# Optimization experiments

Hardware: AMD Instinct MI355X
Metric: run time of the kernel (lower is better)

## Reference

```python
import jax, jax.numpy as jnp
import numpy as np

NUM_HEADS = 16
WINDOW = 256
DIM = 1024


def setup_inputs() -> dict:
    key = jax.random.key(0)
    k1, k2, k3, k4, k5 = jax.random.split(key, 5)
    B, L, D = 2, 2048, DIM
    s = 1.0 / np.sqrt(D)
    return {
        "x": jax.random.normal(k1, (B, L, D), dtype=jnp.float32),
        "in_proj_w": jax.random.uniform(k2, (3 * D, D), dtype=jnp.float32, minval=-s, maxval=s),
        "in_proj_b": jax.random.uniform(k3, (3 * D,), dtype=jnp.float32, minval=-s, maxval=s),
        "out_w": jax.random.uniform(k4, (D, D), dtype=jnp.float32, minval=-s, maxval=s),
        "out_b": jax.random.uniform(k5, (D,), dtype=jnp.float32, minval=-s, maxval=s),
    }


def reference(x, in_proj_w, in_proj_b, out_w, out_b):
    B, L, D = x.shape
    H = NUM_HEADS
    hd = D // H

    # combined qkv projection, as in nn.MultiheadAttention
    qkv = x @ in_proj_w.T + in_proj_b          # [B, L, 3D]
    q, k, v = jnp.split(qkv, 3, axis=-1)
    q = q.reshape(B, L, H, hd).transpose(0, 2, 1, 3)  # [B, H, L, hd]
    k = k.reshape(B, L, H, hd).transpose(0, 2, 1, 3)
    v = v.reshape(B, L, H, hd).transpose(0, 2, 1, 3)

    scale = 1.0 / jnp.sqrt(jnp.asarray(hd, dtype=x.dtype))
    scores = jnp.einsum("bhqd,bhkd->bhqk", q * scale, k)  # [B, H, L, L]

    # sliding-window causal mask: allowed iff i-window < j <= i
    i = jnp.arange(L)[:, None]
    j = jnp.arange(L)[None, :]
    allowed = (j <= i) & (j > i - WINDOW)                  # [L, L]
    scores = jnp.where(allowed[None, None], scores, -jnp.inf)

    attn = jax.nn.softmax(scores, axis=-1)
    out = jnp.einsum("bhqk,bhkd->bhqd", attn, v)           # [B, H, L, hd]
    out = out.transpose(0, 2, 1, 3).reshape(B, L, D)
    return out @ out_w.T + out_b
```

## Files before the change

### kernel.cpp

```cpp
#include <hip/hip_runtime.h>


#define SEQ_L 2048
#define WIN   256

typedef __bf16 bf16x8 __attribute__((ext_vector_type(8)));
typedef float  f32x4  __attribute__((ext_vector_type(4)));

__device__ __forceinline__ unsigned short f32_to_bf16(float f) {
  unsigned int u = __float_as_uint(f);
  u += 0x7FFFu + ((u >> 16) & 1u);
  return (unsigned short)(u >> 16);
}

__device__ __forceinline__ void async16(const unsigned short* g, unsigned short* l) {
  __builtin_amdgcn_global_load_lds(
      (const __attribute__((address_space(1))) unsigned int*)g,
      (__attribute__((address_space(3))) unsigned int*)l, 16, 0, 0);
}

__global__ void cast_all(const float* __restrict__ x,  unsigned short* __restrict__ xo,
                         const float* __restrict__ w1, unsigned short* __restrict__ w1o,
                         const float* __restrict__ w2, unsigned short* __restrict__ w2o) {
  int i = blockIdx.x * 256 + threadIdx.x;
  const float* in; unsigned short* out; int k;
  if (i < 1048576)       { in = x;  out = xo;  k = i; }
  else if (i < 1835008)  { in = w1; out = w1o; k = i - 1048576; }
  else                   { in = w2; out = w2o; k = i - 1835008; }
  float4 v = ((const float4*)in)[k];
  ushort4 o;
  o.x = f32_to_bf16(v.x); o.y = f32_to_bf16(v.y);
  o.z = f32_to_bf16(v.z); o.w = f32_to_bf16(v.w);
  ((ushort4*)out)[k] = o;
}

template<int TBM, int TBN, int MI, int NI, int OUTBF>
__global__ __launch_bounds__(256) void gemm_nt(
    const unsigned short* __restrict__ A,
    const unsigned short* __restrict__ Bt,
    const float* __restrict__ bias,
    void* __restrict__ Cout, int M, int N, int K)
{
  __shared__ unsigned short As[TBM * 64];
  __shared__ unsigned short Bs[TBN * 64];

  const int tid  = threadIdx.x;
  const int lane = tid & 63;
  const int wave = tid >> 6;
  const int wr   = (wave >> 1) * (MI * 16);
  const int wc   = (wave & 1) * (NI * 16);
  const int quad = lane >> 4;
  const int l16  = lane & 15;
  const int lrow = lane >> 3;
  const int scol = (lane & 7) ^ lrow;

  const long m0 = (long)blockIdx.y * TBM;
  const long n0 = (long)blockIdx.x * TBN;

  f32x4 acc[MI][NI];
#pragma unroll
  for (int i = 0; i < MI; ++i)
#pragma unroll
    for (int j = 0; j < NI; ++j)
#pragma unroll
      for (int r = 0; r < 4; ++r) acc[i][j][r] = 0.0f;

  for (int k0 = 0; k0 < K; k0 += 64) {
#pragma unroll
    for (int p = 0; p < TBM / 32; ++p) {
      int rb = wave * (TBM / 4) + p * 8;
      async16(A + (m0 + rb + lrow) * (long)K + k0 + scol * 8, &As[rb * 64]);
    }
#pragma unroll
    for (int p = 0; p < TBN / 32; ++p) {
      int rb = wave * (TBN / 4) + p * 8;
      async16(Bt + (n0 + rb + lrow) * (long)K + k0 + scol * 8, &Bs[rb * 64]);
    }
    __syncthreads();
#pragma unroll
    for (int ks = 0; ks < 2; ++ks) {
      bf16x8 af[MI], bfv[NI];
#pragma unroll
      for (int mi = 0; mi < MI; ++mi) {
        int r = wr + mi * 16 + l16;
        af[mi] = *(const bf16x8*)(&As[r * 64 + ((ks * 4 + quad) ^ (r & 7)) * 8]);
      }
#pragma unroll
      for (int ni = 0; ni < NI; ++ni) {
        int r = wc + ni * 16 + l16;
        bfv[ni] = *(const bf16x8*)(&Bs[r * 64 + ((ks * 4 + quad) ^ (r & 7)) * 8]);
      }
#pragma unroll
      for (int mi = 0; mi < MI; ++mi)
#pragma unroll
        for (int ni = 0; ni < NI; ++ni)
          acc[mi][ni] = __builtin_amdgcn_mfma_f32_16x16x32_bf16(af[mi], bfv[ni], acc[mi][ni], 0, 0, 0);
    }
    __syncthreads();
  }

#pragma unroll
  for (int ni = 0; ni < NI; ++ni) {
    long col = n0 + wc + ni * 16 + l16;
    float bv = bias[col];
#pragma unroll
    for (int mi = 0; mi < MI; ++mi) {
      long rowb = m0 + wr + mi * 16 + quad * 4;
#pragma unroll
      for (int r = 0; r < 4; ++r) {
        float v = acc[mi][ni][r] + bv;
        if (OUTBF) ((unsigned short*)Cout)[(rowb + r) * N + col] = f32_to_bf16(v);
        else       ((float*)Cout)[(rowb + r) * N + col] = v;
      }
    }
  }
}

__global__ __launch_bounds__(256) void attn_kernel(
    const unsigned short* __restrict__ qkv,
    unsigned short* __restrict__ aout)
{
  __shared__ unsigned short Ks[64 * 72];
  __shared__ unsigned short Vt[64 * 72];
  __shared__ unsigned short Ps[4 * 16 * 72];

  const int tid  = threadIdx.x;
  const int w    = tid >> 6;
  const int lane = tid & 63;
  const int quad = lane >> 4;
  const int l16  = lane & 15;

  const int blk = blockIdx.x;
  const int qb  = blk & 15;
  const int h   = (blk >> 4) & 15;
  const int b   = blk >> 8;

  const int  i0 = qb * 128;
  const long rowbase = (long)b * SEQ_L;

  bf16x8 aq[2][2];
#pragma unroll
  for (int sub = 0; sub < 2; ++sub) {
    const unsigned short* qp =
        qkv + (rowbase + i0 + sub * 64 + w * 16 + l16) * 3072 + h * 64 + quad * 8;
    aq[sub][0] = *(const bf16x8*)(qp);
    aq[sub][1] = *(const bf16x8*)(qp + 32);
  }

  f32x4 o[2][4];
  float l_i[2][4];
#pragma unroll
  for (int sub = 0; sub < 2; ++sub)
#pragma unroll
    for (int ni = 0; ni < 4; ++ni)
#pragma unroll
      for (int r = 0; r < 4; ++r) { o[sub][ni][r] = 0.0f; l_i[sub][r] = 0.0f; }

  unsigned short* psw = &Ps[w * 16 * 72];

  const int j_begin = (i0 >= WIN) ? i0 - WIN : 0;

  for (int j0 = j_begin; j0 < i0 + 128; j0 += 64) {
    __syncthreads();
#pragma unroll
    for (int p = 0; p < 2; ++p) {
      int c = p * 256 + tid, row = c >> 3, col8 = c & 7;
      const unsigned short* base = qkv + (rowbase + j0 + row) * 3072 + h * 64 + col8 * 8;
      *(uint4*)(&Ks[row * 72 + col8 * 8]) = *(const uint4*)(base + 1024);
      unsigned short tmp[8];
      *(uint4*)tmp = *(const uint4*)(base + 2048);
      int rsw = row ^ (col8 << 3);
#pragma unroll
      for (int e = 0; e < 8; ++e)
        Vt[(col8 * 8 + e) * 72 + rsw] = tmp[e];
    }
    __syncthreads();

    bf16x8 kf[4][2];
#pragma unroll
    for (int g = 0; g < 4; ++g) {
      kf[g][0] = *(const bf16x8*)(&Ks[(g * 16 + l16) * 72 + quad * 8]);
      kf[g][1] = *(const bf16x8*)(&Ks[(g * 16 + l16) * 72 + 32 + quad * 8]);
    }
    bf16x8 vf[2][4];
#pragma unroll
    for (int kk = 0; kk < 2; ++kk)
#pragma unroll
      for (int ni = 0; ni < 4; ++ni) {
        int d  = ni * 16 + l16;
        int rb = (kk * 32 + quad * 8) ^ (((d >> 3) & 7) << 3);
        vf[kk][ni] = *(const bf16x8*)(&Vt[d * 72 + rb]);
      }

#pragma unroll
    for (int sub = 0; sub < 2; ++sub) {
      const int i0s = i0 + sub * 64 + w * 16;
      if (j0 > i0s + 15) continue;
      if (j0 + 63 + WIN <= i0s) continue;

      f32x4 s[4];
#pragma unroll
      for (int g = 0; g < 4; ++g) {
        f32x4 z;
#pragma unroll
        for (int r = 0; r < 4; ++r) z[r] = 0.0f;
        z = __builtin_amdgcn_mfma_f32_16x16x32_bf16(aq[sub][0], kf[g][0], z, 0, 0, 0);
        z = __builtin_amdgcn_mfma_f32_16x16x32_bf16(aq[sub][1], kf[g][1], z, 0, 0, 0);
        s[g] = z;
      }
#pragma unroll
      for (int g = 0; g < 4; ++g) {
        int j = j0 + g * 16 + l16;
#pragma unroll
        for (int r = 0; r < 4; ++r) {
          int i = i0s + quad * 4 + r;
          bool ok = (j <= i) && (j > i - WIN);
          float e = ok ? __expf(s[g][r] * 0.125f) : 0.0f;
          psw[(quad * 4 + r) * 72 + g * 16 + l16] = f32_to_bf16(e);
          l_i[sub][r] += e;
        }
      }
      asm volatile("s_waitcnt lgkmcnt(0)" ::: "memory");
#pragma unroll
      for (int kk = 0; kk < 2; ++kk) {
        bf16x8 ap = *(const bf16x8*)(&psw[l16 * 72 + kk * 32 + quad * 8]);
#pragma unroll
        for (int ni = 0; ni < 4; ++ni)
          o[sub][ni] = __builtin_amdgcn_mfma_f32_16x16x32_bf16(ap, vf[kk][ni], o[sub][ni], 0, 0, 0);
      }
    }
  }

#pragma unroll
  for (int sub = 0; sub < 2; ++sub)
#pragma unroll
    for (int r = 0; r < 4; ++r) {
      float rs = l_i[sub][r];
      rs += __shfl_xor(rs, 1);
      rs += __shfl_xor(rs, 2);
      rs += __shfl_xor(rs, 4);
      rs += __shfl_xor(rs, 8);
      float inv_l = 1.0f / rs;
      long row = rowbase + i0 + sub * 64 + w * 16 + quad * 4 + r;
#pragma unroll
      for (int ni = 0; ni < 4; ++ni)
        aout[row * 1024 + h * 64 + ni * 16 + l16] = f32_to_bf16(o[sub][ni][r] * inv_l);
    }
}

extern "C" void kernel_launch(void* const* d_in, const int* in_sizes, int n_in,
                              void* d_out, int out_size, void* d_ws, size_t ws_size,
                              hipStream_t stream)
{
  const float* x  = (const float*)d_in[0];
  const float* w1 = (const float*)d_in[1];
  const float* b1 = (const float*)d_in[2];
  const float* w2 = (const float*)d_in[3];
  const float* b2 = (const float*)d_in[4];
  float* out = (float*)d_out;

  char* ws = (char*)d_ws;
  unsigned short* x_bf   = (unsigned short*)(ws);
  unsigned short* w1_bf  = (unsigned short*)(ws + 8388608);
  unsigned short* w2_bf  = (unsigned short*)(ws + 14680064);
  unsigned short* qkv_bf = (unsigned short*)(ws + 16777216);
  unsigned short* at_bf  = (unsigned short*)(ws + 41943040);

  cast_all<<<8192, 256, 0, stream>>>(x, x_bf, w1, w1_bf, w2, w2_bf);

  dim3 g1(3072 / 128, 4096 / 128);
  gemm_nt<128, 128, 4, 4, 1><<<g1, 256, 0, stream>>>(x_bf, w1_bf, b1, qkv_bf, 4096, 3072, 1024);

  attn_kernel<<<512, 256, 0, stream>>>(qkv_bf, at_bf);

  dim3 g2(1024 / 64, 4096 / 64);
  gemm_nt<64, 64, 2, 2, 0><<<g2, 256, 0, stream>>>(at_bf, w2_bf, b2, out, 4096, 1024, 1024);
}
```

Measured before the change: 164.1 us.

## Split-K output GEMM, skip masked tiles, MFMA row sums, exp2 and cheaper bf16 rounding

Replaces the output projection with a new 128x64 kernel that splits K across two wave pairs and reduces the partial sums through shared memory. In attention, fully masked 16-column tiles skip their MFMAs and write zeros, fully visible tiles skip the mask test, exp is computed as exp2 with a folded constant, and the row-sum reduction becomes an MFMA against a vector of ones. The bf16 conversion now rounds half-up instead of round-to-nearest-even. These changes aim to cut ALU, shuffle and GEMM scheduling cost, at the price of slightly different rounding and summing the bf16-rounded probabilities rather than the fp32 ones.

```diff
diff --git a/kernel.cpp b/kernel.cpp
--- a/kernel.cpp
+++ b/kernel.cpp
@@ -8,9 +8,7 @@
 typedef float  f32x4  __attribute__((ext_vector_type(4)));
 
 __device__ __forceinline__ unsigned short f32_to_bf16(float f) {
-  unsigned int u = __float_as_uint(f);
-  u += 0x7FFFu + ((u >> 16) & 1u);
-  return (unsigned short)(u >> 16);
+  return (unsigned short)((__float_as_uint(f) + 0x8000u) >> 16);
 }
 
 __device__ __forceinline__ void async16(const unsigned short* g, unsigned short* l) {
@@ -116,6 +114,101 @@
   }
 }
 
+__global__ __launch_bounds__(256) void gemm_nt_sk(
+    const unsigned short* __restrict__ A,
+    const unsigned short* __restrict__ Bt,
+    const float* __restrict__ bias,
+    float* __restrict__ C, int M, int N, int K)
+{
+  __shared__ unsigned short As[2][128 * 64];
+  __shared__ unsigned short Bs[2][64 * 64];
+
+  const int tid  = threadIdx.x;
+  const int lane = tid & 63;
+  const int wave = tid >> 6;
+  const int half = wave >> 1;
+  const int rh   = wave & 1;
+  const int quad = lane >> 4;
+  const int l16  = lane & 15;
+  const int lrow = lane >> 3;
+  const int scol = (lane & 7) ^ lrow;
+
+  const long m0 = (long)blockIdx.y * 128;
+  const long n0 = (long)blockIdx.x * 64;
+  const int  kh = half * (K / 2);
+
+  f32x4 acc[4][4];
+#pragma unroll
+  for (int i = 0; i < 4; ++i)
+#pragma unroll
+    for (int j = 0; j < 4; ++j)
+#pragma unroll
+      for (int r = 0; r < 4; ++r) acc[i][j][r] = 0.0f;
+
+  for (int it = 0; it < K / 2; it += 64) {
+    const int k0 = kh + it;
+#pragma unroll
+    for (int p = 0; p < 8; ++p) {
+      int rb = rh * 64 + p * 8;
+      async16(A + (m0 + rb + lrow) * (long)K + k0 + scol * 8, &As[half][rb * 64]);
+    }
+#pragma unroll
+    for (int p = 0; p < 4; ++p) {
+      int rb = rh * 32 + p * 8;
+      async16(Bt + (n0 + rb + lrow) * (long)K + k0 + scol * 8, &Bs[half][rb * 64]);
+    }
+    __syncthreads();
+#pragma unroll
+    for (int ks = 0; ks < 2; ++ks) {
+      bf16x8 af[4], bfv[4];
+#pragma unroll
+      for (int mi = 0; mi < 4; ++mi) {
+        int r = rh * 64 + mi * 16 + l16;
+        af[mi] = *(const bf16x8*)(&As[half][r * 64 + ((ks * 4 + quad) ^ (r & 7)) * 8]);
+      }
+#pragma unroll
+      for (int ni = 0; ni < 4; ++ni) {
+        int r = ni * 16 + l16;
+        bfv[ni] = *(const bf16x8*)(&Bs[half][r * 64 + ((ks * 4 + quad) ^ (r & 7)) * 8]);
+      }
+#pragma unroll
+      for (int mi = 0; mi < 4; ++mi)
+#pragma unroll
+        for (int ni = 0; ni < 4; ++ni)
+          acc[mi][ni] = __builtin_amdgcn_mfma_f32_16x16x32_bf16(af[mi], bfv[ni], acc[mi][ni], 0, 0, 0);
+    }
+    __syncthreads();
+  }
+
+  float* Cs = (float*)As;
+  if (half == 1) {
+#pragma unroll
+    for (int mi = 0; mi < 4; ++mi)
+#pragma unroll
+      for (int ni = 0; ni < 4; ++ni) {
+        int slot = ((mi * 4 + ni) * 4 + quad) * 16 + l16;
+        *(f32x4*)&Cs[rh * 4096 + slot * 4] = acc[mi][ni];
+      }
+  }
+  __syncthreads();
+  if (half == 0) {
+#pragma unroll
+    for (int ni = 0; ni < 4; ++ni) {
+      long col = n0 + ni * 16 + l16;
+      float bv = bias[col];
+#pragma unroll
+      for (int mi = 0; mi < 4; ++mi) {
+        int slot = ((mi * 4 + ni) * 4 + quad) * 16 + l16;
+        f32x4 part = *(const f32x4*)&Cs[rh * 4096 + slot * 4];
+        long rowb = m0 + rh * 64 + mi * 16 + quad * 4;
+#pragma unroll
+        for (int r = 0; r < 4; ++r)
+          C[(rowb + r) * N + col] = acc[mi][ni][r] + part[r] + bv;
+      }
+    }
+  }
+}
+
 __global__ __launch_bounds__(256) void attn_kernel(
     const unsigned short* __restrict__ qkv,
     unsigned short* __restrict__ aout)
@@ -137,6 +230,11 @@
 
   const int  i0 = qb * 128;
   const long rowbase = (long)b * SEQ_L;
+  const float C_EXP = 0.18033688f;
+
+  bf16x8 ones;
+#pragma unroll
+  for (int e = 0; e < 8; ++e) ones[e] = (__bf16)1.0f;
 
   bf16x8 aq[2][2];
 #pragma unroll
@@ -147,17 +245,18 @@
     aq[sub][1] = *(const bf16x8*)(qp + 32);
   }
 
-  f32x4 o[2][4];
-  float l_i[2][4];
-#pragma unroll
-  for (int sub = 0; sub < 2; ++sub)
+  f32x4 o[2][4], ol[2];
+#pragma unroll
+  for (int sub = 0; sub < 2; ++sub) {
+#pragma unroll
+    for (int r = 0; r < 4; ++r) ol[sub][r] = 0.0f;
 #pragma unroll
     for (int ni = 0; ni < 4; ++ni)
 #pragma unroll
-      for (int r = 0; r < 4; ++r) { o[sub][ni][r] = 0.0f; l_i[sub][r] = 0.0f; }
+      for (int r = 0; r < 4; ++r) o[sub][ni][r] = 0.0f;
+  }
 
   unsigned short* psw = &Ps[w * 16 * 72];
-
   const int j_begin = (i0 >= WIN) ? i0 - WIN : 0;
 
   for (int j0 = j_begin; j0 < i0 + 128; j0 += 64) {
@@ -198,32 +297,42 @@
       if (j0 > i0s + 15) continue;
       if (j0 + 63 + WIN <= i0s) continue;
 
-      f32x4 s[4];
 #pragma unroll
       for (int g = 0; g < 4; ++g) {
+        const int jmin = j0 + g * 16, jmax = jmin + 15;
+        if (jmin > i0s + 15 || jmax + WIN <= i0s) {
+#pragma unroll
+          for (int r = 0; r < 4; ++r)
+            psw[(quad * 4 + r) * 72 + g * 16 + l16] = 0;
+          continue;
+        }
         f32x4 z;
 #pragma unroll
         for (int r = 0; r < 4; ++r) z[r] = 0.0f;
         z = __builtin_amdgcn_mfma_f32_16x16x32_bf16(aq[sub][0], kf[g][0], z, 0, 0, 0);
         z = __builtin_amdgcn_mfma_f32_16x16x32_bf16(aq[sub][1], kf[g][1], z, 0, 0, 0);
-        s[g] = z;
-      }
-#pragma unroll
-      for (int g = 0; g < 4; ++g) {
-        int j = j0 + g * 16 + l16;
-#pragma unroll
-        for (int r = 0; r < 4; ++r) {
-          int i = i0s + quad * 4 + r;
-          bool ok = (j <= i) && (j > i - WIN);
-          float e = ok ? __expf(s[g][r] * 0.125f) : 0.0f;
-          psw[(quad * 4 + r) * 72 + g * 16 + l16] = f32_to_bf16(e);
-          l_i[sub][r] += e;
+        const bool full = (jmax <= i0s) && (jmin + WIN > i0s + 15);
+        if (full) {
+#pragma unroll
+          for (int r = 0; r < 4; ++r)
+            psw[(quad * 4 + r) * 72 + g * 16 + l16] =
+                f32_to_bf16(__builtin_exp2f(z[r] * C_EXP));
+        } else {
+          const int j = jmin + l16;
+#pragma unroll
+          for (int r = 0; r < 4; ++r) {
+            int i = i0s + quad * 4 + r;
+            bool ok = (j <= i) && (j > i - WIN);
+            float e = ok ? __builtin_exp2f(z[r] * C_EXP) : 0.0f;
+            psw[(quad * 4 + r) * 72 + g * 16 + l16] = f32_to_bf16(e);
+          }
         }
       }
       asm volatile("s_waitcnt lgkmcnt(0)" ::: "memory");
 #pragma unroll
       for (int kk = 0; kk < 2; ++kk) {
         bf16x8 ap = *(const bf16x8*)(&psw[l16 * 72 + kk * 32 + quad * 8]);
+        ol[sub] = __builtin_amdgcn_mfma_f32_16x16x32_bf16(ap, ones, ol[sub], 0, 0, 0);
 #pragma unroll
         for (int ni = 0; ni < 4; ++ni)
           o[sub][ni] = __builtin_amdgcn_mfma_f32_16x16x32_bf16(ap, vf[kk][ni], o[sub][ni], 0, 0, 0);
@@ -235,12 +344,7 @@
   for (int sub = 0; sub < 2; ++sub)
 #pragma unroll
     for (int r = 0; r < 4; ++r) {
-      float rs = l_i[sub][r];
-      rs += __shfl_xor(rs, 1);
-      rs += __shfl_xor(rs, 2);
-      rs += __shfl_xor(rs, 4);
-      rs += __shfl_xor(rs, 8);
-      float inv_l = 1.0f / rs;
+      float inv_l = 1.0f / ol[sub][r];
       long row = rowbase + i0 + sub * 64 + w * 16 + quad * 4 + r;
 #pragma unroll
       for (int ni = 0; ni < 4; ++ni)
@@ -273,6 +377,6 @@
 
   attn_kernel<<<512, 256, 0, stream>>>(qkv_bf, at_bf);
 
-  dim3 g2(1024 / 64, 4096 / 64);
-  gemm_nt<64, 64, 2, 2, 0><<<g2, 256, 0, stream>>>(at_bf, w2_bf, b2, out, 4096, 1024, 1024);
-}
+  dim3 g2(1024 / 64, 4096 / 128);
+  gemm_nt_sk<<<g2, 256, 0, stream>>>(at_bf, w2_bf, b2, out, 4096, 1024, 1024);
+}
```

Result: no change. 165.6 us (+0.9%).

## Skip masked score tiles, use exp2, MFMA row sums, and split QKV GEMM

Applied to the files above, without the earlier changes.

The attention kernel now skips the score MFMAs for 16-column groups that are fully masked and drops per-element mask checks for fully visible groups. It uses exp2 with a folded scale constant and computes softmax row sums with an extra MFMA against a ones vector instead of per-lane accumulation and shuffles. The bf16 rounding is simplified to round-half-up. The QKV projection is split into two launches over halves of the output columns. These changes cut ALU and exp work in the attention inner loop, at the cost of slightly different rounding and one more kernel launch.

```diff
diff --git a/kernel.cpp b/kernel.cpp
--- a/kernel.cpp
+++ b/kernel.cpp
@@ -8,9 +8,7 @@
 typedef float  f32x4  __attribute__((ext_vector_type(4)));
 
 __device__ __forceinline__ unsigned short f32_to_bf16(float f) {
-  unsigned int u = __float_as_uint(f);
-  u += 0x7FFFu + ((u >> 16) & 1u);
-  return (unsigned short)(u >> 16);
+  return (unsigned short)((__float_as_uint(f) + 0x8000u) >> 16);
 }
 
 __device__ __forceinline__ void async16(const unsigned short* g, unsigned short* l) {
@@ -137,6 +135,11 @@
 
   const int  i0 = qb * 128;
   const long rowbase = (long)b * SEQ_L;
+  const float C_EXP = 0.18033688f;
+
+  bf16x8 ones;
+#pragma unroll
+  for (int e = 0; e < 8; ++e) ones[e] = (__bf16)1.0f;
 
   bf16x8 aq[2][2];
 #pragma unroll
@@ -147,17 +150,18 @@
     aq[sub][1] = *(const bf16x8*)(qp + 32);
   }
 
-  f32x4 o[2][4];
-  float l_i[2][4];
-#pragma unroll
-  for (int sub = 0; sub < 2; ++sub)
+  f32x4 o[2][4], ol[2];
+#pragma unroll
+  for (int sub = 0; sub < 2; ++sub) {
+#pragma unroll
+    for (int r = 0; r < 4; ++r) ol[sub][r] = 0.0f;
 #pragma unroll
     for (int ni = 0; ni < 4; ++ni)
 #pragma unroll
-      for (int r = 0; r < 4; ++r) { o[sub][ni][r] = 0.0f; l_i[sub][r] = 0.0f; }
+      for (int r = 0; r < 4; ++r) o[sub][ni][r] = 0.0f;
+  }
 
   unsigned short* psw = &Ps[w * 16 * 72];
-
   const int j_begin = (i0 >= WIN) ? i0 - WIN : 0;
 
   for (int j0 = j_begin; j0 < i0 + 128; j0 += 64) {
@@ -198,32 +202,42 @@
       if (j0 > i0s + 15) continue;
       if (j0 + 63 + WIN <= i0s) continue;
 
-      f32x4 s[4];
 #pragma unroll
       for (int g = 0; g < 4; ++g) {
+        const int jmin = j0 + g * 16, jmax = jmin + 15;
+        if (jmin > i0s + 15 || jmax + WIN <= i0s) {
+#pragma unroll
+          for (int r = 0; r < 4; ++r)
+            psw[(quad * 4 + r) * 72 + g * 16 + l16] = 0;
+          continue;
+        }
         f32x4 z;
 #pragma unroll
         for (int r = 0; r < 4; ++r) z[r] = 0.0f;
         z = __builtin_amdgcn_mfma_f32_16x16x32_bf16(aq[sub][0], kf[g][0], z, 0, 0, 0);
         z = __builtin_amdgcn_mfma_f32_16x16x32_bf16(aq[sub][1], kf[g][1], z, 0, 0, 0);
-        s[g] = z;
-      }
-#pragma unroll
-      for (int g = 0; g < 4; ++g) {
-        int j = j0 + g * 16 + l16;
-#pragma unroll
-        for (int r = 0; r < 4; ++r) {
-          int i = i0s + quad * 4 + r;
-          bool ok = (j <= i) && (j > i - WIN);
-          float e = ok ? __expf(s[g][r] * 0.125f) : 0.0f;
-          psw[(quad * 4 + r) * 72 + g * 16 + l16] = f32_to_bf16(e);
-          l_i[sub][r] += e;
+        const bool full = (jmax <= i0s) && (jmin + WIN > i0s + 15);
+        if (full) {
+#pragma unroll
+          for (int r = 0; r < 4; ++r)
+            psw[(quad * 4 + r) * 72 + g * 16 + l16] =
+                f32_to_bf16(__builtin_exp2f(z[r] * C_EXP));
+        } else {
+          const int j = jmin + l16;
+#pragma unroll
+          for (int r = 0; r < 4; ++r) {
+            int i = i0s + quad * 4 + r;
+            bool ok = (j <= i) && (j > i - WIN);
+            float e = ok ? __builtin_exp2f(z[r] * C_EXP) : 0.0f;
+            psw[(quad * 4 + r) * 72 + g * 16 + l16] = f32_to_bf16(e);
+          }
         }
       }
       asm volatile("s_waitcnt lgkmcnt(0)" ::: "memory");
 #pragma unroll
       for (int kk = 0; kk < 2; ++kk) {
         bf16x8 ap = *(const bf16x8*)(&psw[l16 * 72 + kk * 32 + quad * 8]);
+        ol[sub] = __builtin_amdgcn_mfma_f32_16x16x32_bf16(ap, ones, ol[sub], 0, 0, 0);
 #pragma unroll
         for (int ni = 0; ni < 4; ++ni)
           o[sub][ni] = __builtin_amdgcn_mfma_f32_16x16x32_bf16(ap, vf[kk][ni], o[sub][ni], 0, 0, 0);
@@ -235,12 +249,7 @@
   for (int sub = 0; sub < 2; ++sub)
 #pragma unroll
     for (int r = 0; r < 4; ++r) {
-      float rs = l_i[sub][r];
-      rs += __shfl_xor(rs, 1);
-      rs += __shfl_xor(rs, 2);
-      rs += __shfl_xor(rs, 4);
-      rs += __shfl_xor(rs, 8);
-      float inv_l = 1.0f / rs;
+      float inv_l = 1.0f / ol[sub][r];
       long row = rowbase + i0 + sub * 64 + w * 16 + quad * 4 + r;
 #pragma unroll
       for (int ni = 0; ni < 4; ++ni)
@@ -268,8 +277,11 @@
 
   cast_all<<<8192, 256, 0, stream>>>(x, x_bf, w1, w1_bf, w2, w2_bf);
 
-  dim3 g1(3072 / 128, 4096 / 128);
-  gemm_nt<128, 128, 4, 4, 1><<<g1, 256, 0, stream>>>(x_bf, w1_bf, b1, qkv_bf, 4096, 3072, 1024);
+  dim3 g1(1536 / 128, 4096 / 128);
+  gemm_nt<128, 128, 4, 4, 1><<<g1, 256, 0, stream>>>(
+      x_bf, w1_bf, b1, qkv_bf, 4096, 3072, 1024);
+  gemm_nt<128, 128, 4, 4, 1><<<g1, 256, 0, stream>>>(
+      x_bf, w1_bf + 1536 * 1024, b1 + 1536, qkv_bf + 1536, 4096, 3072, 1024);
 
   attn_kernel<<<512, 256, 0, stream>>>(qkv_bf, at_bf);
 
```

Result: slower. 172.8 us (+5.3%).
